# Kernel tuning notes

Hardware: AMD Instinct MI355X
Metric: run time of the kernel (lower is better)

## Reference

```python
import jax, jax.numpy as jnp
import numpy as np

B, H, W, C = 2, 128, 128, 192
HEADS = 6
HD = C // HEADS
WS = 16
OWIN = int(WS * 0.5) + WS          # 24
PAD = (OWIN - WS) // 2             # 4
NQ = WS * WS
NK = OWIN * OWIN
EPS = 1e-6
HID = ((int(C * 2.667) + 7) // 8) * 8  # 512


def _rel_pos_index():
    cq = np.stack(np.meshgrid(np.arange(WS), np.arange(WS), indexing='ij')).reshape(2, -1)
    ck = np.stack(np.meshgrid(np.arange(OWIN), np.arange(OWIN), indexing='ij')).reshape(2, -1)
    rel = (ck[:, None, :] - cq[:, :, None]).transpose(1, 2, 0).astype(np.int64)  # (nq, nk, 2)
    rel[:, :, 0] += WS - 1
    rel[:, :, 1] += WS - 1
    rel[:, :, 0] *= WS + OWIN - 1
    return rel.sum(-1)  # (nq, nk)

RPI = jnp.asarray(_rel_pos_index())


def setup_inputs() -> dict:
    key = jax.random.key(0)
    ks = jax.random.split(key, 16)
    def w(k, shape, s=0.02):
        return jax.random.normal(k, shape, jnp.float32) * s
    return {
        'x': jax.random.normal(ks[0], (B, H * W, C), jnp.float32),
        'qkv_w': w(ks[1], (3 * C, C)), 'qkv_b': jnp.zeros((3 * C,), jnp.float32),
        'proj_w': w(ks[2], (C, C)), 'proj_b': jnp.zeros((C,), jnp.float32),
        'rpb': w(ks[3], ((WS + OWIN - 1) ** 2, HEADS)),
        'n1_w': jnp.ones((C,), jnp.float32), 'n1_b': jnp.zeros((C,), jnp.float32),
        'ls1': jnp.full((C,), 1e-6, jnp.float32),
        'n2_w': jnp.ones((C,), jnp.float32), 'n2_b': jnp.zeros((C,), jnp.float32),
        'ls2': jnp.full((C,), 1e-6, jnp.float32),
        'fcgv_w': w(ks[4], (2 * HID, C)), 'fcgv_b': jnp.zeros((2 * HID,), jnp.float32),
        'dw_w': w(ks[5], (HID, 1, 3, 3)), 'dw_b': jnp.zeros((HID,), jnp.float32),
        'dwd_w': w(ks[6], (HID, 1, 3, 3)), 'dwd_b': jnp.zeros((HID,), jnp.float32),
        'dil_scale': w(ks[7], (1,), 0.1),
        'fco_w': w(ks[8], (C, HID)), 'fco_b': jnp.zeros((C,), jnp.float32),
    }


def _iln(x, wgt, bias):
    # spatially-holistic LN: stats over (L, C); returns normed x and residual scale
    xf = x.astype(jnp.float32)
    mean = xf.mean(axis=(1, 2), keepdims=True)
    var = ((xf - mean) ** 2).mean(axis=(1, 2), keepdims=True)
    std = jnp.sqrt(var + EPS)
    scale = jnp.minimum(std, 2.0)  # std_ema buffer initialized to 1.0 (eval path)
    xn = (xf - mean) / scale
    return (xn * wgt + bias).astype(x.dtype), scale


def _oca(x, qkv_w, qkv_b, proj_w, proj_b, rpb):
    b = x.shape[0]
    nh, nw = H // WS, W // WS
    nwin = b * nh * nw
    qkv = x @ qkv_w.T + qkv_b
    q, k, v = jnp.split(qkv, 3, axis=-1)
    # non-overlapping query windows: (nwin, heads, nq, hd)
    qw = q.reshape(b, nh, WS, nw, WS, C).transpose(0, 1, 3, 2, 4, 5)
    qw = qw.reshape(nwin, NQ, HEADS, HD).transpose(0, 2, 1, 3)
    # overlapping K/V windows via unfold(kernel=OWIN, stride=WS, pad=PAD)
    kv = jnp.concatenate([k, v], axis=-1).reshape(b, H, W, 2 * C).transpose(0, 3, 1, 2)
    kvp = jnp.pad(kv, ((0, 0), (0, 0), (PAD, PAD), (PAD, PAD)))
    ih = (jnp.arange(nh) * WS)[:, None] + jnp.arange(OWIN)[None, :]
    iw = (jnp.arange(nw) * WS)[:, None] + jnp.arange(OWIN)[None, :]
    kvw = kvp[:, :, ih][:, :, :, :, iw]               # (b, 2C, nh, owin, nw, owin)
    kvw = kvw.transpose(0, 2, 4, 3, 5, 1).reshape(nwin, NK, 2 * C)
    kw = kvw[..., :C].reshape(nwin, NK, HEADS, HD).transpose(0, 2, 1, 3)
    vw = kvw[..., C:].reshape(nwin, NK, HEADS, HD).transpose(0, 2, 1, 3)
    bias = rpb[RPI].transpose(2, 0, 1)                # (heads, nq, nk)
    logits = jnp.einsum('whqd,whkd->whqk', qw, kw) * (HD ** -0.5) + bias
    attn = jax.nn.softmax(logits, axis=-1)
    out = jnp.einsum('whqk,whkd->whqd', attn, vw)
    out = out.transpose(0, 2, 1, 3).reshape(nwin, NQ, C) @ proj_w.T + proj_b
    # window reverse -> (b, H*W, C)
    out = out.reshape(b, nh, nw, WS, WS, C).transpose(0, 1, 3, 2, 4, 5).reshape(b, H * W, C)
    return out


def _dw(x, wgt, bias, dil):
    y = jax.lax.conv_general_dilated(x, wgt, (1, 1), [(dil, dil), (dil, dil)],
                                     rhs_dilation=(dil, dil), feature_group_count=HID)
    return y + bias[None, :, None, None]


def _ffn(x, fcgv_w, fcgv_b, dw_w, dw_b, dwd_w, dwd_b, dil_scale, fco_w, fco_b):
    gv = x @ fcgv_w.T + fcgv_b
    g, val = jnp.split(gv, 2, axis=-1)
    h = jax.nn.silu(g) * val
    h = h.transpose(0, 2, 1).reshape(-1, HID, H, W)
    h = _dw(h, dw_w, dw_b, 1)
    h = h + dil_scale[0] * _dw(h, dwd_w, dwd_b, 2)
    h = h.reshape(-1, HID, H * W).transpose(0, 2, 1)
    return h @ fco_w.T + fco_b


def reference(x, qkv_w, qkv_b, proj_w, proj_b, rpb, n1_w, n1_b, ls1, n2_w, n2_b, ls2,
              fcgv_w, fcgv_b, dw_w, dw_b, dwd_w, dwd_b, dil_scale, fco_w, fco_b):
    xn, std1 = _iln(x, n1_w, n1_b)
    x = x + std1 * (ls1 * _oca(xn, qkv_w, qkv_b, proj_w, proj_b, rpb))
    xn2, std2 = _iln(x, n2_w, n2_b)
    x = x + std2 * (ls2 * _ffn(xn2, fcgv_w, fcgv_b, dw_w, dw_b, dwd_w, dwd_b, dil_scale, fco_w, fco_b))
    return x
```

## Files before the change

### kernel.cpp

```cpp
#include <hip/hip_runtime.h>

#define DI __device__ __forceinline__

typedef __attribute__((ext_vector_type(8))) short bh8;
typedef __attribute__((ext_vector_type(4))) float fx4;
typedef __attribute__((ext_vector_type(16))) float fx16;

DI short f2bf(float f) {
  unsigned u = __builtin_bit_cast(unsigned, f);
  u += 0x7FFFu + ((u >> 16) & 1u);
  return (short)(u >> 16);
}
DI float bf2f(short s) {
  unsigned u = ((unsigned)(unsigned short)s) << 16;
  return __builtin_bit_cast(float, u);
}
DI fx4 mfma16(bh8 a, bh8 b, fx4 c) {
  return __builtin_amdgcn_mfma_f32_16x16x32_bf16(a, b, c, 0, 0, 0);
}
DI fx16 mfma32(bh8 a, bh8 b, fx16 c) {
  return __builtin_amdgcn_mfma_f32_32x32x16_bf16(a, b, c, 0, 0, 0);
}
DI fx4 fzero() { fx4 z = {0.f, 0.f, 0.f, 0.f}; return z; }

DI bh8 pack8(const float* src) {
  fx4 v0 = *(const fx4*)src;
  fx4 v1 = *(const fx4*)(src + 4);
  bh8 pk;
#pragma unroll
  for (int j = 0; j < 4; j++) { pk[j] = f2bf(v0[j]); pk[j + 4] = f2bf(v1[j]); }
  return pk;
}
DI bh8 pack8_aff(const float* src, const float* affc) {
  fx4 v0 = *(const fx4*)src;
  fx4 v1 = *(const fx4*)(src + 4);
  bh8 pk;
#pragma unroll
  for (int j = 0; j < 4; j++) {
    pk[j]     = f2bf(v0[j] * affc[2 * j]       + affc[2 * j + 1]);
    pk[j + 4] = f2bf(v1[j] * affc[2 * (j + 4)] + affc[2 * (j + 4) + 1]);
  }
  return pk;
}

__global__ __launch_bounds__(256) void iln_partial(const float* __restrict__ x,
                                                   float* __restrict__ part) {
  const int blk = blockIdx.x, tid = threadIdx.x;
  const fx4* p = (const fx4*)(x + (size_t)blk * 12288);
  float s = 0.f, s2 = 0.f;
#pragma unroll
  for (int i = 0; i < 12; i++) {
    fx4 v = p[i * 256 + tid];
    s  += v[0] + v[1] + v[2] + v[3];
    s2 += v[0] * v[0] + v[1] * v[1] + v[2] * v[2] + v[3] * v[3];
  }
  __shared__ float sm[512];
  sm[tid] = s; sm[256 + tid] = s2;
  __syncthreads();
  for (int st = 128; st > 0; st >>= 1) {
    if (tid < st) { sm[tid] += sm[tid + st]; sm[256 + tid] += sm[256 + tid + st]; }
    __syncthreads();
  }
  if (tid == 0) { part[blk * 2] = sm[0]; part[blk * 2 + 1] = sm[256]; }
}

__global__ __launch_bounds__(256) void iln_final(const float* __restrict__ part,
                                                 const float* __restrict__ w,
                                                 const float* __restrict__ bias,
                                                 float* __restrict__ aff,
                                                 float* __restrict__ st) {
  const int b = blockIdx.x, tid = threadIdx.x;
  __shared__ float sm[512];
  sm[tid]       = part[(b * 256 + tid) * 2];
  sm[256 + tid] = part[(b * 256 + tid) * 2 + 1];
  __syncthreads();
  for (int s = 128; s > 0; s >>= 1) {
    if (tid < s) { sm[tid] += sm[tid + s]; sm[256 + tid] += sm[256 + tid + s]; }
    __syncthreads();
  }
  const float invn = 1.f / 3145728.f;
  float mean = sm[0] * invn;
  float var  = sm[256] * invn - mean * mean;
  float scale = fminf(sqrtf(var + 1e-6f), 2.f);
  if (tid < 192) {
    float a = w[tid] / scale;
    aff[(b * 192 + tid) * 2]     = a;
    aff[(b * 192 + tid) * 2 + 1] = bias[tid] - mean * a;
  }
  if (tid == 0) { st[b * 2] = mean; st[b * 2 + 1] = scale; }
}

__global__ __launch_bounds__(256) void cvt_w(const float* __restrict__ qkv_w,
                                             const float* __restrict__ proj_w,
                                             const float* __restrict__ fcgv_w,
                                             const float* __restrict__ fco_w,
                                             short* __restrict__ wbuf) {
  int t = blockIdx.x * 256 + threadIdx.x;
  int off = t * 8;
  const float* src;
  if (off < 110592)       src = qkv_w + off;
  else if (off < 147456)  src = proj_w + (off - 110592);
  else if (off < 344064)  src = fcgv_w + (off - 147456);
  else                    src = fco_w + (off - 344064);
  *(bh8*)(wbuf + off) = pack8(src);
}

__global__ __launch_bounds__(256) void cvt_aff(const float* __restrict__ src,
                                               const float* __restrict__ aff,
                                               short* __restrict__ dst) {
  int t = blockIdx.x * 256 + threadIdx.x;
  int row = t / 24;
  int c0 = (t - row * 24) * 8;
  const float* affp = aff + (row >> 14) * 384 + c0 * 2;
  *(bh8*)(dst + (size_t)t * 8) = pack8_aff(src + (size_t)row * 192 + c0, affp);
}

__global__ __launch_bounds__(256) void bias_gen(const float* __restrict__ rpb,
                                                short* __restrict__ bt) {
  int t = blockIdx.x * 256 + threadIdx.x;
  int lane = t & 63;
  int u = t >> 6;
  int qi = u & 1; u >>= 1;
  int ki = u & 1; u >>= 1;
  int kc = u % 9; u = u / 9;
  int w = u & 3, head = u >> 2;
  int c = lane & 31, hi = lane >> 5;
  int q = w * 64 + qi * 32 + c;
  int qterm = (q >> 4) * 39 + (q & 15);
  short o[16];
#pragma unroll
  for (int r = 0; r < 16; r++) {
    int k = kc * 64 + ki * 32 + (r & 3) + 8 * (r >> 2) + 4 * hi;
    int ky = (k * 2731) >> 16;
    int kx = k - ky * 24;
    int idx = ky * 39 + kx + 600 - qterm;
    o[r] = f2bf(rpb[idx * 6 + head] * 5.656854249492381f);
  }
  *(bh8*)(bt + (size_t)t * 16)     = *(bh8*)&o[0];
  *(bh8*)(bt + (size_t)t * 16 + 8) = *(bh8*)&o[8];
}

__global__ __launch_bounds__(256) void gemm_qkv(const short* __restrict__ xn,
                                                const short* __restrict__ wq,
                                                const float* __restrict__ wb,
                                                short* __restrict__ qb,
                                                short* __restrict__ kb,
                                                short* __restrict__ vb) {
  __shared__ short As[128 * 40];
  __shared__ short Bs[96 * 40];
  const int m0 = blockIdx.x * 128, by = blockIdx.y, n0 = by * 96;
  const int tid = threadIdx.x, wid = tid >> 6, lane = tid & 63;
  const int g = lane >> 4, h = lane & 15;
  const int wm = wid >> 1, wn = wid & 1;
  fx4 acc[4][3];
#pragma unroll
  for (int i = 0; i < 4; i++)
#pragma unroll
    for (int j = 0; j < 3; j++) acc[i][j] = fzero();

  for (int kt = 0; kt < 6; kt++) {
    const int k0 = kt * 32;
#pragma unroll
    for (int i = 0; i < 2; i++) {
      int ch = tid + i * 256;
      int row = ch >> 2, sl = ch & 3;
      *(bh8*)&As[row * 40 + sl * 8] = *(const bh8*)(xn + (size_t)(m0 + row) * 192 + k0 + sl * 8);
    }
    {
      int row = tid >> 2, sl = tid & 3;
      *(bh8*)&Bs[row * 40 + sl * 8] = *(const bh8*)(wq + (size_t)(n0 + row) * 192 + k0 + sl * 8);
      int ch = tid + 256;
      if (ch < 384) {
        row = ch >> 2; sl = ch & 3;
        *(bh8*)&Bs[row * 40 + sl * 8] = *(const bh8*)(wq + (size_t)(n0 + row) * 192 + k0 + sl * 8);
      }
    }
    __syncthreads();
    bh8 af[4];
#pragma unroll
    for (int mi = 0; mi < 4; mi++)
      af[mi] = *(bh8*)&As[(wm * 64 + mi * 16 + h) * 40 + g * 8];
#pragma unroll
    for (int ni = 0; ni < 3; ni++) {
      bh8 bf = *(bh8*)&Bs[(wn * 48 + ni * 16 + h) * 40 + g * 8];
#pragma unroll
      for (int mi = 0; mi < 4; mi++) acc[mi][ni] = mfma16(af[mi], bf, acc[mi][ni]);
    }
    __syncthreads();
  }
  const int seg = by >> 1;
  short* dst = (seg == 0) ? qb : (seg == 1 ? kb : vb);
  const int colbase = (by & 1) * 96;
#pragma unroll
  for (int mi = 0; mi < 4; mi++)
#pragma unroll
    for (int ni = 0; ni < 3; ni++)
#pragma unroll
      for (int r = 0; r < 4; r++) {
        int row = m0 + wm * 64 + mi * 16 + g * 4 + r;
        int col = colbase + wn * 48 + ni * 16 + h;
        dst[(size_t)row * 192 + col] = f2bf(acc[mi][ni][r] + wb[seg * 192 + col]);
      }
}

__global__ __launch_bounds__(256, 3) void attn_kernel(const short* __restrict__ qb,
                                                      const short* __restrict__ kb,
                                                      const short* __restrict__ vb,
                                                      const short* __restrict__ bt,
                                                      short* __restrict__ ao) {
  __shared__ short K_lds[64 * 40];
  __shared__ short Vt_lds[32 * 72];
  __shared__ float l_lds[256];
  const int tid = threadIdx.x;
  const int win = blockIdx.x, head = blockIdx.y;
  const int b = win >> 6, wy = (win >> 3) & 7, wx = win & 7;
  const int w = tid >> 6, lane = tid & 63, c = lane & 31, hi = lane >> 5;
  const float SCALE = 0.1767766952966369f;

  bh8 qf[2][2];
#pragma unroll
  for (int qi = 0; qi < 2; qi++) {
    int ql = w * 64 + qi * 32 + c;
    size_t gl = (size_t)(b * 16384 + (wy * 16 + (ql >> 4)) * 128 + wx * 16 + (ql & 15));
#pragma unroll
    for (int ds = 0; ds < 2; ds++)
      qf[qi][ds] = *(const bh8*)(qb + gl * 192 + head * 32 + ds * 16 + hi * 8);
  }
  float l_run[2] = {0.f, 0.f};
  fx16 out[2];
#pragma unroll
  for (int r = 0; r < 16; r++) { out[0][r] = 0.f; out[1][r] = 0.f; }

  const short* btw = bt + (size_t)(head * 4 + w) * 36864;

  const int kl_a = tid >> 2, part_a = tid & 3;
  const int kl_b = tid & 63, hg_b = tid >> 6;

  for (int kc = 0; kc < 9; kc++) {
    __syncthreads();
    {
      int key = kc * 64 + kl_a;
      int ky = key / 24, kx = key - ky * 24;
      int py = wy * 16 - 4 + ky, px = wx * 16 - 4 + kx;
      bh8 kv = {};
      if ((unsigned)py < 128u && (unsigned)px < 128u)
        kv = *(const bh8*)(kb + ((size_t)(b * 16384 + py * 128 + px)) * 192 + head * 32 + part_a * 8);
      *(bh8*)&K_lds[kl_a * 40 + part_a * 8] = kv;

      int key2 = kc * 64 + kl_b;
      int ky2 = key2 / 24, kx2 = key2 - ky2 * 24;
      int py2 = wy * 16 - 4 + ky2, px2 = wx * 16 - 4 + kx2;
      bh8 vv = {};
      if ((unsigned)py2 < 128u && (unsigned)px2 < 128u)
        vv = *(const bh8*)(vb + ((size_t)(b * 16384 + py2 * 128 + px2)) * 192 + head * 32 + hg_b * 8);
#pragma unroll
      for (int j = 0; j < 8; j++) Vt_lds[(hg_b * 8 + j) * 72 + kl_b] = vv[j];
    }
    __syncthreads();

#pragma unroll
    for (int ki = 0; ki < 2; ki++) {
      fx16 st[2];
#pragma unroll
      for (int qi = 0; qi < 2; qi++) {
        const short* bp = btw + (((kc * 2 + ki) * 2 + qi) * 64 + lane) * 16;
        int4 b0 = *(const int4*)bp;
        int4 b1 = *(const int4*)(bp + 8);
#pragma unroll
        for (int d2 = 0; d2 < 4; d2++) {
          unsigned u0 = ((const unsigned*)&b0)[d2];
          unsigned u1 = ((const unsigned*)&b1)[d2];
          st[qi][d2 * 2]     = __builtin_bit_cast(float, u0 << 16);
          st[qi][d2 * 2 + 1] = __builtin_bit_cast(float, u0 & 0xffff0000u);
          st[qi][8 + d2 * 2]     = __builtin_bit_cast(float, u1 << 16);
          st[qi][8 + d2 * 2 + 1] = __builtin_bit_cast(float, u1 & 0xffff0000u);
        }
      }
#pragma unroll
      for (int ds = 0; ds < 2; ds++) {
        bh8 kf = *(bh8*)&K_lds[(ki * 32 + c) * 40 + ds * 16 + hi * 8];
        st[0] = mfma32(kf, qf[0][ds], st[0]);
        st[1] = mfma32(kf, qf[1][ds], st[1]);
      }
#pragma unroll
      for (int qi = 0; qi < 2; qi++) {
        float s = 0.f;
#pragma unroll
        for (int r = 0; r < 16; r++) {
          float p = __expf(st[qi][r] * SCALE);
          st[qi][r] = p;
          s += p;
        }
        l_run[qi] += s;
      }
      int dwq[2][2][4];
#pragma unroll
      for (int qi = 0; qi < 2; qi++)
#pragma unroll
        for (int k1 = 0; k1 < 2; k1++)
#pragma unroll
          for (int p01 = 0; p01 < 2; p01++) {
            int rA = 2 * p01 + 8 * k1;
            int A, Bv;
            asm("v_cvt_pk_bf16_f32 %0, %1, %2" : "=v"(A)  : "v"(st[qi][rA]),     "v"(st[qi][rA + 1]));
            asm("v_cvt_pk_bf16_f32 %0, %1, %2" : "=v"(Bv) : "v"(st[qi][rA + 4]), "v"(st[qi][rA + 5]));
            int Ax = __shfl_xor(A, 32);
            int Bx = __shfl_xor(Bv, 32);
            dwq[qi][k1][p01]     = hi ? Bx : A;
            dwq[qi][k1][p01 + 2] = hi ? Bv : Ax;
          }
#pragma unroll
      for (int k1 = 0; k1 < 2; k1++) {
        bh8 bv2 = *(bh8*)&Vt_lds[c * 72 + (ki * 2 + k1) * 16 + hi * 8];
#pragma unroll
        for (int qi = 0; qi < 2; qi++) {
          int4 t4 = {dwq[qi][k1][0], dwq[qi][k1][1], dwq[qi][k1][2], dwq[qi][k1][3]};
          out[qi] = mfma32(__builtin_bit_cast(bh8, t4), bv2, out[qi]);
        }
      }
    }
  }
#pragma unroll
  for (int qi = 0; qi < 2; qi++) {
    float lp = l_run[qi] + __shfl_xor(l_run[qi], 32);
    l_lds[w * 64 + qi * 32 + c] = 1.f / lp;
  }
  __syncthreads();
#pragma unroll
  for (int qi = 0; qi < 2; qi++)
#pragma unroll
    for (int r = 0; r < 16; r++) {
      int row = (r & 3) + 8 * (r >> 2) + 4 * hi;
      float val = out[qi][r] * l_lds[w * 64 + qi * 32 + row];
      int ql = w * 64 + qi * 32 + row;
      ao[((size_t)(win * 256 + ql)) * 192 + head * 32 + c] = f2bf(val);
    }
}

__global__ __launch_bounds__(256) void gemm_proj(const short* __restrict__ ao,
                                                 const short* __restrict__ wp,
                                                 const float* __restrict__ wb,
                                                 const float* __restrict__ x,
                                                 const float* __restrict__ ls1,
                                                 const float* __restrict__ st,
                                                 float* __restrict__ x1,
                                                 float* __restrict__ part2) {
  __shared__ short As[128 * 40];
  __shared__ short Bs[96 * 40];
  const int m0 = blockIdx.x * 128, by = blockIdx.y, n0 = by * 96;
  const int tid = threadIdx.x, wid = tid >> 6, lane = tid & 63;
  const int g = lane >> 4, h = lane & 15;
  const int wm = wid >> 1, wn = wid & 1;
  fx4 acc[4][3];
#pragma unroll
  for (int i = 0; i < 4; i++)
#pragma unroll
    for (int j = 0; j < 3; j++) acc[i][j] = fzero();

  for (int kt = 0; kt < 6; kt++) {
    const int k0 = kt * 32;
#pragma unroll
    for (int i = 0; i < 2; i++) {
      int ch = tid + i * 256;
      int row = ch >> 2, sl = ch & 3;
      *(bh8*)&As[row * 40 + sl * 8] = *(const bh8*)(ao + (size_t)(m0 + row) * 192 + k0 + sl * 8);
    }
    {
      int row = tid >> 2, sl = tid & 3;
      *(bh8*)&Bs[row * 40 + sl * 8] = *(const bh8*)(wp + (size_t)(n0 + row) * 192 + k0 + sl * 8);
      int ch = tid + 256;
      if (ch < 384) {
        row = ch >> 2; sl = ch & 3;
        *(bh8*)&Bs[row * 40 + sl * 8] = *(const bh8*)(wp + (size_t)(n0 + row) * 192 + k0 + sl * 8);
      }
    }
    __syncthreads();
    bh8 af[4];
#pragma unroll
    for (int mi = 0; mi < 4; mi++)
      af[mi] = *(bh8*)&As[(wm * 64 + mi * 16 + h) * 40 + g * 8];
#pragma unroll
    for (int ni = 0; ni < 3; ni++) {
      bh8 bf = *(bh8*)&Bs[(wn * 48 + ni * 16 + h) * 40 + g * 8];
#pragma unroll
      for (int mi = 0; mi < 4; mi++) acc[mi][ni] = mfma16(af[mi], bf, acc[mi][ni]);
    }
    __syncthreads();
  }
  float ps = 0.f, ps2 = 0.f;
#pragma unroll
  for (int mi = 0; mi < 4; mi++)
#pragma unroll
    for (int ni = 0; ni < 3; ni++)
#pragma unroll
      for (int r = 0; r < 4; r++) {
        int grow = m0 + wm * 64 + mi * 16 + g * 4 + r;
        int win = grow >> 8, q = grow & 255;
        int bb = win >> 6, wy = (win >> 3) & 7, wxx = win & 7;
        int l = (wy * 16 + (q >> 4)) * 128 + wxx * 16 + (q & 15);
        int col = n0 + wn * 48 + ni * 16 + h;
        size_t di = ((size_t)(bb * 16384 + l)) * 192 + col;
        float s1 = st[bb * 2 + 1];
        float val = x[di] + s1 * ls1[col] * (acc[mi][ni][r] + wb[col]);
        x1[di] = val;
        ps += val;
        ps2 += val * val;
      }
  float* red = (float*)As;
  red[tid] = ps; red[256 + tid] = ps2;
  __syncthreads();
  for (int s = 128; s > 0; s >>= 1) {
    if (tid < s) { red[tid] += red[tid + s]; red[256 + tid] += red[256 + tid + s]; }
    __syncthreads();
  }
  if (tid == 0) {
    int pi = blockIdx.x * 2 + by;
    part2[pi * 2] = red[0];
    part2[pi * 2 + 1] = red[256];
  }
}

__global__ __launch_bounds__(256) void gemm_fcgv(const short* __restrict__ x1n,
                                                 const short* __restrict__ wg,
                                                 const float* __restrict__ wb,
                                                 short* __restrict__ hp) {
  __shared__ short smem[128 * 40 + 128 * 40];
  short* As = smem;
  short* Bs = smem + 128 * 40;
  const int m0 = blockIdx.x * 128, n0 = blockIdx.y * 64;
  const int b = m0 >> 14, l0 = m0 & 16383;
  const int tid = threadIdx.x, wid = tid >> 6, lane = tid & 63;
  const int g = lane >> 4, h = lane & 15;
  const int wm = wid >> 1, wn = wid & 1;
  fx4 accg[4][2], accv[4][2];
#pragma unroll
  for (int i = 0; i < 4; i++)
#pragma unroll
    for (int j = 0; j < 2; j++) { accg[i][j] = fzero(); accv[i][j] = fzero(); }

  for (int kt = 0; kt < 6; kt++) {
    const int k0 = kt * 32;
#pragma unroll
    for (int i = 0; i < 2; i++) {
      int ch = tid + i * 256;
      int row = ch >> 2, sl = ch & 3;
      *(bh8*)&As[row * 40 + sl * 8] = *(const bh8*)(x1n + (size_t)(m0 + row) * 192 + k0 + sl * 8);
    }
#pragma unroll
    for (int i = 0; i < 2; i++) {
      int ch = tid + i * 256;
      int row = ch >> 2, sl = ch & 3;
      int wrow = (row < 64) ? (n0 + row) : (512 + n0 + row - 64);
      *(bh8*)&Bs[row * 40 + sl * 8] = *(const bh8*)(wg + (size_t)wrow * 192 + k0 + sl * 8);
    }
    __syncthreads();
    bh8 af[4];
#pragma unroll
    for (int mi = 0; mi < 4; mi++)
      af[mi] = *(bh8*)&As[(wm * 64 + mi * 16 + h) * 40 + g * 8];
#pragma unroll
    for (int ni = 0; ni < 2; ni++) {
      bh8 bg = *(bh8*)&Bs[(wn * 32 + ni * 16 + h) * 40 + g * 8];
      bh8 bv = *(bh8*)&Bs[(64 + wn * 32 + ni * 16 + h) * 40 + g * 8];
#pragma unroll
      for (int mi = 0; mi < 4; mi++) {
        accg[mi][ni] = mfma16(af[mi], bg, accg[mi][ni]);
        accv[mi][ni] = mfma16(af[mi], bv, accv[mi][ni]);
      }
    }
    __syncthreads();
  }
  short hs[4][2][4];
#pragma unroll
  for (int mi = 0; mi < 4; mi++)
#pragma unroll
    for (int ni = 0; ni < 2; ni++)
#pragma unroll
      for (int r = 0; r < 4; r++) {
        int colg = n0 + wn * 32 + ni * 16 + h;
        float gv = accg[mi][ni][r] + wb[colg];
        float vv = accv[mi][ni][r] + wb[512 + colg];
        hs[mi][ni][r] = f2bf(gv / (1.f + __expf(-gv)) * vv);
      }
  short* T = smem;
#pragma unroll
  for (int mi = 0; mi < 4; mi++)
#pragma unroll
    for (int ni = 0; ni < 2; ni++)
#pragma unroll
      for (int r = 0; r < 4; r++) {
        int cc = wn * 32 + ni * 16 + h;
        int rl = wm * 64 + mi * 16 + g * 4 + r;
        T[cc * 136 + rl] = hs[mi][ni][r];
      }
  __syncthreads();
#pragma unroll
  for (int i = 0; i < 4; i++) {
    int ch = tid + i * 256;
    int cc = ch >> 4, lg = ch & 15;
    bh8 v = *(bh8*)&T[cc * 136 + lg * 8];
    *(bh8*)(hp + (((size_t)(b * 512 + n0 + cc)) << 14) + l0 + lg * 8) = v;
  }
}

__global__ __launch_bounds__(256, 2) void dw_fused(const short* __restrict__ in,
                                                   const float* __restrict__ w1,
                                                   const float* __restrict__ b1,
                                                   const float* __restrict__ w2,
                                                   const float* __restrict__ b2,
                                                   const float* __restrict__ dsc,
                                                   short* __restrict__ outp) {
  __shared__ short P[136 * 128];
  __shared__ short D[136 * 128];
  const int p = blockIdx.x, c = p & 511;
  const int tid = threadIdx.x;
#pragma unroll
  for (int i = 0; i < 8; i++) {
    int gs = i * 256 + tid;
    int yy = gs >> 4, sl = gs & 15;
    bh8 v = *(const bh8*)(in + ((size_t)p << 14) + gs * 8);
    *(bh8*)&P[yy * 136 + sl * 8] = v;
  }
  float k1[9], k2[9];
#pragma unroll
  for (int j = 0; j < 9; j++) { k1[j] = w1[c * 9 + j]; k2[j] = w2[c * 9 + j]; }
  const float bias1 = b1[c], bias2 = b2[c], ds = dsc[0];
  const int y = tid >> 1, hf = tid & 1;
  __syncthreads();

#pragma unroll
  for (int g = 0; g < 8; g++) {
    const int x0 = hf * 64 + g * 8;
    float acc[8];
#pragma unroll
    for (int i = 0; i < 8; i++) acc[i] = bias1;
#pragma unroll
    for (int ky = 0; ky < 3; ky++) {
      int yy = y + ky - 1;
      if ((unsigned)yy < 128u) {
        const short* row = &P[yy * 136];
        float f[10];
        bh8 v = *(const bh8*)&row[x0];
#pragma unroll
        for (int j = 0; j < 8; j++) f[j + 1] = bf2f(v[j]);
        f[0] = (x0 == 0) ? 0.f : bf2f(row[x0 - 1]);
        f[9] = (x0 == 120) ? 0.f : bf2f(row[x0 + 8]);
        float w0 = k1[ky * 3], wA = k1[ky * 3 + 1], wB = k1[ky * 3 + 2];
#pragma unroll
        for (int i = 0; i < 8; i++) acc[i] += f[i] * w0 + f[i + 1] * wA + f[i + 2] * wB;
      }
    }
    bh8 pk;
#pragma unroll
    for (int i = 0; i < 8; i++) pk[i] = f2bf(acc[i]);
    *(bh8*)&D[y * 136 + x0] = pk;
  }
  __syncthreads();

#pragma unroll
  for (int g = 0; g < 8; g++) {
    const int x0 = hf * 64 + g * 8;
    float acc[8], center[8];
#pragma unroll
    for (int i = 0; i < 8; i++) acc[i] = bias2;
#pragma unroll
    for (int ky = 0; ky < 3; ky++) {
      int yy = y + (ky - 1) * 2;
      if ((unsigned)yy < 128u) {
        const short* row = &D[yy * 136];
        float f[12];
        bh8 v = *(const bh8*)&row[x0];
#pragma unroll
        for (int j = 0; j < 8; j++) f[j + 2] = bf2f(v[j]);
        if (x0 == 0) { f[0] = 0.f; f[1] = 0.f; }
        else {
          unsigned lp = *(const unsigned*)&row[x0 - 2];
          f[0] = __builtin_bit_cast(float, lp << 16);
          f[1] = __builtin_bit_cast(float, lp & 0xffff0000u);
        }
        if (x0 == 120) { f[10] = 0.f; f[11] = 0.f; }
        else {
          unsigned rp = *(const unsigned*)&row[x0 + 8];
          f[10] = __builtin_bit_cast(float, rp << 16);
          f[11] = __builtin_bit_cast(float, rp & 0xffff0000u);
        }
        float w0 = k2[ky * 3], wA = k2[ky * 3 + 1], wB = k2[ky * 3 + 2];
#pragma unroll
        for (int i = 0; i < 8; i++) acc[i] += f[i] * w0 + f[i + 2] * wA + f[i + 4] * wB;
        if (ky == 1) {
#pragma unroll
          for (int i = 0; i < 8; i++) center[i] = f[i + 2];
        }
      }
    }
    bh8 pk;
#pragma unroll
    for (int i = 0; i < 8; i++) pk[i] = f2bf(center[i] + ds * acc[i]);
    *(bh8*)(outp + ((size_t)p << 14) + y * 128 + x0) = pk;
  }
}

__global__ __launch_bounds__(256) void gemm_fco(const short* __restrict__ h2,
                                                const short* __restrict__ wo,
                                                const float* __restrict__ wb,
                                                const float* __restrict__ x1,
                                                const float* __restrict__ ls2,
                                                const float* __restrict__ st,
                                                float* __restrict__ out) {
  __shared__ short As[128 * 40];
  __shared__ short Bs[96 * 40];
  const int m0 = blockIdx.x * 128, by = blockIdx.y, n0 = by * 96;
  const int b = m0 >> 14, l0 = m0 & 16383;
  const int tid = threadIdx.x, wid = tid >> 6, lane = tid & 63;
  const int g = lane >> 4, h = lane & 15;
  const int wm = wid >> 1, wn = wid & 1;
  fx4 acc[4][3];
#pragma unroll
  for (int i = 0; i < 4; i++)
#pragma unroll
    for (int j = 0; j < 3; j++) acc[i][j] = fzero();

  for (int kt = 0; kt < 16; kt++) {
    const int k0 = kt * 32;
#pragma unroll
    for (int i = 0; i < 2; i++) {
      int ch = tid + i * 256;
      int cc = ch & 31, lgrp = ch >> 5;
      bh8 v = *(const bh8*)(h2 + (((size_t)(b * 512 + k0 + cc)) << 14) + l0 + lgrp * 8);
#pragma unroll
      for (int j = 0; j < 8; j++) As[(lgrp * 8 + j) * 40 + cc] = v[j];
    }
    {
      int row = tid >> 2, sl = tid & 3;
      *(bh8*)&Bs[row * 40 + sl * 8] = *(const bh8*)(wo + (size_t)(n0 + row) * 512 + k0 + sl * 8);
      int ch = tid + 256;
      if (ch < 384) {
        row = ch >> 2; sl = ch & 3;
        *(bh8*)&Bs[row * 40 + sl * 8] = *(const bh8*)(wo + (size_t)(n0 + row) * 512 + k0 + sl * 8);
      }
    }
    __syncthreads();
    bh8 af[4];
#pragma unroll
    for (int mi = 0; mi < 4; mi++)
      af[mi] = *(bh8*)&As[(wm * 64 + mi * 16 + h) * 40 + g * 8];
#pragma unroll
    for (int ni = 0; ni < 3; ni++) {
      bh8 bf = *(bh8*)&Bs[(wn * 48 + ni * 16 + h) * 40 + g * 8];
#pragma unroll
      for (int mi = 0; mi < 4; mi++) acc[mi][ni] = mfma16(af[mi], bf, acc[mi][ni]);
    }
    __syncthreads();
  }
  float s2 = st[b * 2 + 1];
#pragma unroll
  for (int mi = 0; mi < 4; mi++)
#pragma unroll
    for (int ni = 0; ni < 3; ni++)
#pragma unroll
      for (int r = 0; r < 4; r++) {
        int row = m0 + wm * 64 + mi * 16 + g * 4 + r;
        int col = n0 + wn * 48 + ni * 16 + h;
        size_t di = (size_t)row * 192 + col;
        out[di] = x1[di] + s2 * ls2[col] * (acc[mi][ni][r] + wb[col]);
      }
}

extern "C" void kernel_launch(void* const* d_in, const int* in_sizes, int n_in,
                              void* d_out, int out_size, void* d_ws, size_t ws_size,
                              hipStream_t stream) {
  const float* x      = (const float*)d_in[0];
  const float* qkv_w  = (const float*)d_in[1];
  const float* qkv_b  = (const float*)d_in[2];
  const float* proj_w = (const float*)d_in[3];
  const float* proj_b = (const float*)d_in[4];
  const float* rpb    = (const float*)d_in[5];
  const float* n1_w   = (const float*)d_in[6];
  const float* n1_b   = (const float*)d_in[7];
  const float* ls1    = (const float*)d_in[8];
  const float* n2_w   = (const float*)d_in[9];
  const float* n2_b   = (const float*)d_in[10];
  const float* ls2    = (const float*)d_in[11];
  const float* fcgv_w = (const float*)d_in[12];
  const float* fcgv_b = (const float*)d_in[13];
  const float* dw_w   = (const float*)d_in[14];
  const float* dw_b   = (const float*)d_in[15];
  const float* dwd_w  = (const float*)d_in[16];
  const float* dwd_b  = (const float*)d_in[17];
  const float* dil    = (const float*)d_in[18];
  const float* fco_w  = (const float*)d_in[19];
  const float* fco_b  = (const float*)d_in[20];
  float* out = (float*)d_out;
  char* ws = (char*)d_ws;

  short* wbuf = (short*)(ws + 0);
  short* wq = wbuf;
  short* wp = wbuf + 110592;
  short* wg = wbuf + 147456;
  short* wo = wbuf + 344064;
  float* part  = (float*)(ws + 884736);
  float* aff1  = (float*)(ws + 888832);
  float* aff2  = (float*)(ws + 890368);
  float* st1   = (float*)(ws + 891904);
  float* st2   = (float*)(ws + 891968);
  float* part2 = (float*)(ws + 892032);
  short* xn  = (short*)(ws + 1048576);
  short* bt  = (short*)(ws + 13631488);
  short* qb  = (short*)(ws + 15400960);
  short* kb  = (short*)(ws + 27983872);
  short* vb  = (short*)(ws + 40566784);
  short* ao  = (short*)(ws + 53149696);
  float* x1  = (float*)(ws + 1048576);
  short* x1n = (short*)(ws + 26214400);
  short* hp  = (short*)(ws + 40566784);

  cvt_w<<<216, 256, 0, stream>>>(qkv_w, proj_w, fcgv_w, fco_w, wbuf);
  iln_partial<<<512, 256, 0, stream>>>(x, part);
  iln_final<<<2, 256, 0, stream>>>(part, n1_w, n1_b, aff1, st1);
  cvt_aff<<<3072, 256, 0, stream>>>(x, aff1, xn);
  bias_gen<<<216, 256, 0, stream>>>(rpb, bt);
  gemm_qkv<<<dim3(256, 6), 256, 0, stream>>>(xn, wq, qkv_b, qb, kb, vb);
  attn_kernel<<<dim3(128, 6), 256, 0, stream>>>(qb, kb, vb, bt, ao);
  gemm_proj<<<dim3(256, 2), 256, 0, stream>>>(ao, wp, proj_b, x, ls1, st1, x1, part2);
  iln_final<<<2, 256, 0, stream>>>(part2, n2_w, n2_b, aff2, st2);
  cvt_aff<<<3072, 256, 0, stream>>>(x1, aff2, x1n);
  gemm_fcgv<<<dim3(256, 8), 256, 0, stream>>>(x1n, wg, fcgv_b, hp);
  dw_fused<<<1024, 256, 0, stream>>>(hp, dw_w, dw_b, dwd_w, dwd_b, dil, hp);
  gemm_fco<<<dim3(256, 2), 256, 0, stream>>>(hp, wo, fco_b, x1, ls2, st2, out);
}
```

Baseline: 189.9 us.

## Double-buffer attention K/V, fold softmax scale into K, fp32 bias, packed LDS stores

The attention kernel now double-buffers K and V tiles in LDS, prefetching the next chunk into registers before computing on the current one. This removes one barrier per iteration and hides global load latency. The softmax scale and log2(e) are folded into K at the QKV GEMM and into the relative-position bias, so exp2 can be used directly, and the bias table is stored as fp32 to drop the unpack work. It also uses permlane32_swap instead of shuffles where available, and the fco GEMM packs pairs of channels into 32-bit LDS stores. The costs are extra LDS, more registers, and a bias table twice as large, which adds global traffic.

Result: no change. 189.7 us (-0.1%).

```diff
diff --git a/kernel.cpp b/kernel.cpp
--- a/kernel.cpp
+++ b/kernel.cpp
@@ -22,6 +22,14 @@
   return __builtin_amdgcn_mfma_f32_32x32x16_bf16(a, b, c, 0, 0, 0);
 }
 DI fx4 fzero() { fx4 z = {0.f, 0.f, 0.f, 0.f}; return z; }
+
+DI float fexp2(float x) {
+#if __has_builtin(__builtin_amdgcn_exp2f)
+  return __builtin_amdgcn_exp2f(x);
+#else
+  return exp2f(x);
+#endif
+}
 
 DI bh8 pack8(const float* src) {
   fx4 v0 = *(const fx4*)src;
@@ -116,28 +124,35 @@
 }
 
 __global__ __launch_bounds__(256) void bias_gen(const float* __restrict__ rpb,
-                                                short* __restrict__ bt) {
+                                                float* __restrict__ btf) {
   int t = blockIdx.x * 256 + threadIdx.x;
   int lane = t & 63;
   int u = t >> 6;
-  int qi = u & 1; u >>= 1;
-  int ki = u & 1; u >>= 1;
-  int kc = u % 9; u = u / 9;
-  int w = u & 3, head = u >> 2;
+  int qi = u & 1; int u2 = u >> 1;
+  int ki = u2 & 1; u2 >>= 1;
+  int kc = u2 % 9; u2 = u2 / 9;
+  int w = u2 & 3, head = u2 >> 2;
   int c = lane & 31, hi = lane >> 5;
   int q = w * 64 + qi * 32 + c;
   int qterm = (q >> 4) * 39 + (q & 15);
-  short o[16];
+  (void)ki; (void)kc;
+  float o[16];
 #pragma unroll
   for (int r = 0; r < 16; r++) {
-    int k = kc * 64 + ki * 32 + (r & 3) + 8 * (r >> 2) + 4 * hi;
-    int ky = (k * 2731) >> 16;
-    int kx = k - ky * 24;
+    int k = (u & 0x3c) ? 0 : 0;
+    (void)k;
+    int kk = ((u >> 2) % 9) * 64 + ((u >> 1) & 1) * 32 + (r & 3) + 8 * (r >> 2) + 4 * hi;
+    int ky = (kk * 2731) >> 16;
+    int kx = kk - ky * 24;
     int idx = ky * 39 + kx + 600 - qterm;
-    o[r] = f2bf(rpb[idx * 6 + head] * 5.656854249492381f);
-  }
-  *(bh8*)(bt + (size_t)t * 16)     = *(bh8*)&o[0];
-  *(bh8*)(bt + (size_t)t * 16 + 8) = *(bh8*)&o[8];
+    o[r] = rpb[idx * 6 + head] * 1.4426950408889634f;
+  }
+  fx4* dst = (fx4*)btf;
+#pragma unroll
+  for (int j = 0; j < 4; j++) {
+    fx4 v = {o[4 * j], o[4 * j + 1], o[4 * j + 2], o[4 * j + 3]};
+    dst[((size_t)u * 4 + j) * 64 + lane] = v;
+  }
 }
 
 __global__ __launch_bounds__(256) void gemm_qkv(const short* __restrict__ xn,
@@ -190,6 +205,7 @@
   }
   const int seg = by >> 1;
   short* dst = (seg == 0) ? qb : (seg == 1 ? kb : vb);
+  const float sc = (seg == 1) ? 0.25503486f : 1.0f;
   const int colbase = (by & 1) * 96;
 #pragma unroll
   for (int mi = 0; mi < 4; mi++)
@@ -199,23 +215,22 @@
       for (int r = 0; r < 4; r++) {
         int row = m0 + wm * 64 + mi * 16 + g * 4 + r;
         int col = colbase + wn * 48 + ni * 16 + h;
-        dst[(size_t)row * 192 + col] = f2bf(acc[mi][ni][r] + wb[seg * 192 + col]);
+        dst[(size_t)row * 192 + col] = f2bf((acc[mi][ni][r] + wb[seg * 192 + col]) * sc);
       }
 }
 
 __global__ __launch_bounds__(256, 3) void attn_kernel(const short* __restrict__ qb,
                                                       const short* __restrict__ kb,
                                                       const short* __restrict__ vb,
-                                                      const short* __restrict__ bt,
+                                                      const float* __restrict__ btf,
                                                       short* __restrict__ ao) {
-  __shared__ short K_lds[64 * 40];
-  __shared__ short Vt_lds[32 * 72];
+  __shared__ short K_lds[2][64 * 40];
+  __shared__ short Vt_lds[2][32 * 72];
   __shared__ float l_lds[256];
   const int tid = threadIdx.x;
   const int win = blockIdx.x, head = blockIdx.y;
   const int b = win >> 6, wy = (win >> 3) & 7, wx = win & 7;
   const int w = tid >> 6, lane = tid & 63, c = lane & 31, hi = lane >> 5;
-  const float SCALE = 0.1767766952966369f;
 
   bh8 qf[2][2];
 #pragma unroll
@@ -231,54 +246,62 @@
 #pragma unroll
   for (int r = 0; r < 16; r++) { out[0][r] = 0.f; out[1][r] = 0.f; }
 
-  const short* btw = bt + (size_t)(head * 4 + w) * 36864;
+  const fx4* btf4 = (const fx4*)btf;
+  const int hw9 = (head * 4 + w) * 9;
 
   const int kl_a = tid >> 2, part_a = tid & 3;
   const int kl_b = tid & 63, hg_b = tid >> 6;
 
+  auto load_kv = [&](int kc, bh8& kr, bh8& vr) {
+    int key = kc * 64 + kl_a;
+    int ky = key / 24, kx = key - ky * 24;
+    int py = wy * 16 - 4 + ky, px = wx * 16 - 4 + kx;
+    bh8 kv = {};
+    if ((unsigned)py < 128u && (unsigned)px < 128u)
+      kv = *(const bh8*)(kb + ((size_t)(b * 16384 + py * 128 + px)) * 192 + head * 32 + part_a * 8);
+    kr = kv;
+    int key2 = kc * 64 + kl_b;
+    int ky2 = key2 / 24, kx2 = key2 - ky2 * 24;
+    int py2 = wy * 16 - 4 + ky2, px2 = wx * 16 - 4 + kx2;
+    bh8 vv = {};
+    if ((unsigned)py2 < 128u && (unsigned)px2 < 128u)
+      vv = *(const bh8*)(vb + ((size_t)(b * 16384 + py2 * 128 + px2)) * 192 + head * 32 + hg_b * 8);
+    vr = vv;
+  };
+
+  {
+    bh8 k0r, v0r;
+    load_kv(0, k0r, v0r);
+    *(bh8*)&K_lds[0][kl_a * 40 + part_a * 8] = k0r;
+#pragma unroll
+    for (int j = 0; j < 8; j++) Vt_lds[0][(hg_b * 8 + j) * 72 + kl_b] = v0r[j];
+  }
+  int cur = 0;
+
   for (int kc = 0; kc < 9; kc++) {
-    __syncthreads();
-    {
-      int key = kc * 64 + kl_a;
-      int ky = key / 24, kx = key - ky * 24;
-      int py = wy * 16 - 4 + ky, px = wx * 16 - 4 + kx;
-      bh8 kv = {};
-      if ((unsigned)py < 128u && (unsigned)px < 128u)
-        kv = *(const bh8*)(kb + ((size_t)(b * 16384 + py * 128 + px)) * 192 + head * 32 + part_a * 8);
-      *(bh8*)&K_lds[kl_a * 40 + part_a * 8] = kv;
-
-      int key2 = kc * 64 + kl_b;
-      int ky2 = key2 / 24, kx2 = key2 - ky2 * 24;
-      int py2 = wy * 16 - 4 + ky2, px2 = wx * 16 - 4 + kx2;
-      bh8 vv = {};
-      if ((unsigned)py2 < 128u && (unsigned)px2 < 128u)
-        vv = *(const bh8*)(vb + ((size_t)(b * 16384 + py2 * 128 + px2)) * 192 + head * 32 + hg_b * 8);
-#pragma unroll
-      for (int j = 0; j < 8; j++) Vt_lds[(hg_b * 8 + j) * 72 + kl_b] = vv[j];
-    }
-    __syncthreads();
-
+    bh8 kn, vn;
+    if (kc < 8) load_kv(kc + 1, kn, vn);
+    __syncthreads();
+
+    const fx4* base_kc = btf4 + (size_t)(hw9 + kc) * 1024 + lane;
 #pragma unroll
     for (int ki = 0; ki < 2; ki++) {
       fx16 st[2];
 #pragma unroll
       for (int qi = 0; qi < 2; qi++) {
-        const short* bp = btw + (((kc * 2 + ki) * 2 + qi) * 64 + lane) * 16;
-        int4 b0 = *(const int4*)bp;
-        int4 b1 = *(const int4*)(bp + 8);
-#pragma unroll
-        for (int d2 = 0; d2 < 4; d2++) {
-          unsigned u0 = ((const unsigned*)&b0)[d2];
-          unsigned u1 = ((const unsigned*)&b1)[d2];
-          st[qi][d2 * 2]     = __builtin_bit_cast(float, u0 << 16);
-          st[qi][d2 * 2 + 1] = __builtin_bit_cast(float, u0 & 0xffff0000u);
-          st[qi][8 + d2 * 2]     = __builtin_bit_cast(float, u1 << 16);
-          st[qi][8 + d2 * 2 + 1] = __builtin_bit_cast(float, u1 & 0xffff0000u);
+        const fx4* bp = base_kc + (ki * 2 + qi) * 256;
+        fx4 b0 = bp[0], b1 = bp[64], b2 = bp[128], b3 = bp[192];
+#pragma unroll
+        for (int m = 0; m < 4; m++) {
+          st[qi][m]      = b0[m];
+          st[qi][4 + m]  = b1[m];
+          st[qi][8 + m]  = b2[m];
+          st[qi][12 + m] = b3[m];
         }
       }
 #pragma unroll
       for (int ds = 0; ds < 2; ds++) {
-        bh8 kf = *(bh8*)&K_lds[(ki * 32 + c) * 40 + ds * 16 + hi * 8];
+        bh8 kf = *(bh8*)&K_lds[cur][(ki * 32 + c) * 40 + ds * 16 + hi * 8];
         st[0] = mfma32(kf, qf[0][ds], st[0]);
         st[1] = mfma32(kf, qf[1][ds], st[1]);
       }
@@ -287,7 +310,7 @@
         float s = 0.f;
 #pragma unroll
         for (int r = 0; r < 16; r++) {
-          float p = __expf(st[qi][r] * SCALE);
+          float p = fexp2(st[qi][r]);
           st[qi][r] = p;
           s += p;
         }
@@ -304,14 +327,20 @@
             int A, Bv;
             asm("v_cvt_pk_bf16_f32 %0, %1, %2" : "=v"(A)  : "v"(st[qi][rA]),     "v"(st[qi][rA + 1]));
             asm("v_cvt_pk_bf16_f32 %0, %1, %2" : "=v"(Bv) : "v"(st[qi][rA + 4]), "v"(st[qi][rA + 5]));
+#if __has_builtin(__builtin_amdgcn_permlane32_swap)
+            auto pr = __builtin_amdgcn_permlane32_swap((unsigned)A, (unsigned)Bv, false, false);
+            dwq[qi][k1][p01]     = (int)pr[0];
+            dwq[qi][k1][p01 + 2] = (int)pr[1];
+#else
             int Ax = __shfl_xor(A, 32);
             int Bx = __shfl_xor(Bv, 32);
             dwq[qi][k1][p01]     = hi ? Bx : A;
             dwq[qi][k1][p01 + 2] = hi ? Bv : Ax;
+#endif
           }
 #pragma unroll
       for (int k1 = 0; k1 < 2; k1++) {
-        bh8 bv2 = *(bh8*)&Vt_lds[c * 72 + (ki * 2 + k1) * 16 + hi * 8];
+        bh8 bv2 = *(bh8*)&Vt_lds[cur][c * 72 + (ki * 2 + k1) * 16 + hi * 8];
 #pragma unroll
         for (int qi = 0; qi < 2; qi++) {
           int4 t4 = {dwq[qi][k1][0], dwq[qi][k1][1], dwq[qi][k1][2], dwq[qi][k1][3]};
@@ -319,6 +348,12 @@
         }
       }
     }
+    if (kc < 8) {
+      *(bh8*)&K_lds[cur ^ 1][kl_a * 40 + part_a * 8] = kn;
+#pragma unroll
+      for (int j = 0; j < 8; j++) Vt_lds[cur ^ 1][(hg_b * 8 + j) * 72 + kl_b] = vn[j];
+    }
+    cur ^= 1;
   }
 #pragma unroll
   for (int qi = 0; qi < 2; qi++) {
@@ -614,6 +649,7 @@
   const int tid = threadIdx.x, wid = tid >> 6, lane = tid & 63;
   const int g = lane >> 4, h = lane & 15;
   const int wm = wid >> 1, wn = wid & 1;
+  const int cp = tid & 15, lg = tid >> 4;
   fx4 acc[4][3];
 #pragma unroll
   for (int i = 0; i < 4; i++)
@@ -622,13 +658,15 @@
 
   for (int kt = 0; kt < 16; kt++) {
     const int k0 = kt * 32;
-#pragma unroll
-    for (int i = 0; i < 2; i++) {
-      int ch = tid + i * 256;
-      int cc = ch & 31, lgrp = ch >> 5;
-      bh8 v = *(const bh8*)(h2 + (((size_t)(b * 512 + k0 + cc)) << 14) + l0 + lgrp * 8);
-#pragma unroll
-      for (int j = 0; j < 8; j++) As[(lgrp * 8 + j) * 40 + cc] = v[j];
+    {
+      const short* basep = h2 + (((size_t)(b * 512 + k0 + 2 * cp)) << 14) + l0 + lg * 8;
+      bh8 v0 = *(const bh8*)basep;
+      bh8 v1 = *(const bh8*)(basep + 16384);
+#pragma unroll
+      for (int j = 0; j < 8; j++) {
+        unsigned pkv = (unsigned)(unsigned short)v0[j] | (((unsigned)(unsigned short)v1[j]) << 16);
+        *(unsigned*)&As[(lg * 8 + j) * 40 + 2 * cp] = pkv;
+      }
     }
     {
       int row = tid >> 2, sl = tid & 3;
@@ -705,22 +743,22 @@
   float* st2   = (float*)(ws + 891968);
   float* part2 = (float*)(ws + 892032);
   short* xn  = (short*)(ws + 1048576);
-  short* bt  = (short*)(ws + 13631488);
-  short* qb  = (short*)(ws + 15400960);
-  short* kb  = (short*)(ws + 27983872);
-  short* vb  = (short*)(ws + 40566784);
-  short* ao  = (short*)(ws + 53149696);
+  float* btf = (float*)(ws + 13631488);
+  short* qb  = (short*)(ws + 17301504);
+  short* kb  = (short*)(ws + 29884416);
+  short* vb  = (short*)(ws + 42467328);
+  short* ao  = (short*)(ws + 55050240);
   float* x1  = (float*)(ws + 1048576);
   short* x1n = (short*)(ws + 26214400);
-  short* hp  = (short*)(ws + 40566784);
+  short* hp  = (short*)(ws + 42467328);
 
   cvt_w<<<216, 256, 0, stream>>>(qkv_w, proj_w, fcgv_w, fco_w, wbuf);
   iln_partial<<<512, 256, 0, stream>>>(x, part);
   iln_final<<<2, 256, 0, stream>>>(part, n1_w, n1_b, aff1, st1);
   cvt_aff<<<3072, 256, 0, stream>>>(x, aff1, xn);
-  bias_gen<<<216, 256, 0, stream>>>(rpb, bt);
+  bias_gen<<<216, 256, 0, stream>>>(rpb, btf);
   gemm_qkv<<<dim3(256, 6), 256, 0, stream>>>(xn, wq, qkv_b, qb, kb, vb);
-  attn_kernel<<<dim3(128, 6), 256, 0, stream>>>(qb, kb, vb, bt, ao);
+  attn_kernel<<<dim3(128, 6), 256, 0, stream>>>(qb, kb, vb, btf, ao);
   gemm_proj<<<dim3(256, 2), 256, 0, stream>>>(ao, wp, proj_b, x, ls1, st1, x1, part2);
   iln_final<<<2, 256, 0, stream>>>(part2, n2_w, n2_b, aff2, st2);
   cvt_aff<<<3072, 256, 0, stream>>>(x1, aff2, x1n);
```
